# Optimization experiments

Hardware: AMD Instinct MI355X
Metric: run time of the kernel (lower is better)

## Reference

```python
import jax, jax.numpy as jnp
import numpy as np

B, S, M = 1, 1024, 1024          # batch, seq, hidden
H, D, KV = 16, 64, 8             # q heads, head dim, kv heads (kv hardcoded=8)
G = H // KV                      # gqa groups
FF = 3072                        # expert/shared mlp inner dim (hardcoded)
E, K = 64, 8                     # experts, topk (hardcoded)
CAP = 2 * K * S * B // E         # static expert capacity (>= dynamic max -> no drops)
RMS_EPS = 1e-6
F32_EPS = 1.1920929e-07          # torch.finfo(float32).eps


def _rms(x, w, eps=RMS_EPS):
    v = jnp.mean(x * x, axis=-1, keepdims=True)
    return w * (x * jax.lax.rsqrt(v + eps))


def _rotate_half(x):
    d = x.shape[-1] // 2
    return jnp.concatenate([-x[..., d:], x[..., :d]], axis=-1)


def _mlp(x, gu_w, dn_w):
    gu = x @ gu_w                       # [..., 2*FF]
    x1, x2 = gu[..., :FF], gu[..., FF:]
    return (x1 * jax.nn.silu(x2)) @ dn_w


def _topkgating(logits):
    # logits: [T, E] fp32
    gates = jax.nn.softmax(logits, axis=1)
    topv, topi = jax.lax.top_k(gates, K)                 # [T, K]
    gates_s = jnp.clip(jnp.sum(topv, axis=1, keepdims=True), F32_EPS)
    router_probs = gates / gates_s                        # [T, E]
    # priority: cumsum of one-hot over flattened (K, T) order, matching torch
    idx_flat = topi.T.reshape(-1)                         # [K*T]
    mask = jax.nn.one_hot(idx_flat, E, dtype=jnp.int32)   # [K*T, E]
    prio = jnp.cumsum(mask, axis=0) * mask - 1            # [K*T, E]
    prio = prio.reshape(K, -1, E).transpose(1, 0, 2).max(axis=1)  # [T, E]
    valid = (prio >= 0) & (prio < CAP)
    prio = jnp.where(valid, prio, 0)
    dispatch = jax.nn.one_hot(prio, CAP, dtype=jnp.float32) * valid[..., None]  # [T,E,C]
    combine = router_probs[..., None] * dispatch                                 # [T,E,C]
    return combine, dispatch


def setup_inputs() -> dict:
    key = jax.random.key(0)
    ks = jax.random.split(key, 10)
    sc = 0.02
    inv_freq = 1.0 / (10000.0 ** (jnp.arange(0, D, 2, dtype=jnp.float32) / D))
    t = jnp.arange(S, dtype=jnp.float32)
    freqs = jnp.outer(t, inv_freq)                        # [S, D/2]
    emb = jnp.concatenate([freqs, freqs], axis=-1)        # [S, D]
    cos = jnp.broadcast_to(jnp.cos(emb), (B, S, D))
    sin = jnp.broadcast_to(jnp.sin(emb), (B, S, D))
    return {
        'hidden_states': jax.random.normal(ks[0], (B, S, M), jnp.float32),
        'cos': cos,
        'sin': sin,
        'ln1_w': jnp.ones((M,), jnp.float32),
        'ln2_w': jnp.ones((M,), jnp.float32),
        'qkv_w': jax.random.normal(ks[1], (M, (H + 2 * KV) * D), jnp.float32) * sc,
        'o_w': jax.random.normal(ks[2], (H * D, M), jnp.float32) * sc,
        'qn_w': jnp.ones((D,), jnp.float32),
        'kn_w': jnp.ones((D,), jnp.float32),
        'shared_gu_w': jax.random.normal(ks[3], (M, 2 * FF), jnp.float32) * sc,
        'shared_dn_w': jax.random.normal(ks[4], (FF, M), jnp.float32) * sc,
        'gate_w': jax.random.normal(ks[5], (M, E), jnp.float32) * sc,
        'expert_gu_w': jax.random.normal(ks[6], (E, M, 2 * FF), jnp.float32) * sc,
        'expert_dn_w': jax.random.normal(ks[7], (E, FF, M), jnp.float32) * sc,
    }


def reference(hidden_states, cos, sin, ln1_w, ln2_w, qkv_w, o_w, qn_w, kn_w,
              shared_gu_w, shared_dn_w, gate_w, expert_gu_w, expert_dn_w):
    # ---- attention block ----
    hn = _rms(hidden_states, ln1_w)                       # input layernorm
    qkv = (hn @ qkv_w).reshape(B, S, KV, G + 2, D)
    q = qkv[..., :G, :].reshape(B, S, H, D).transpose(0, 2, 1, 3)   # [B,H,S,D]
    k = qkv[..., G, :].transpose(0, 2, 1, 3)                        # [B,KV,S,D]
    v = qkv[..., G + 1, :].transpose(0, 2, 1, 3)                    # [B,KV,S,D]
    c, s_ = cos[:, None], sin[:, None]                    # [B,1,S,D]
    q = q * c + _rotate_half(q) * s_
    k = k * c + _rotate_half(k) * s_
    q = _rms(q, qn_w)
    k = _rms(k, kn_w)
    k = jnp.repeat(k, G, axis=1)                          # GQA expand -> [B,H,S,D]
    v = jnp.repeat(v, G, axis=1)
    scores = jnp.einsum('bhqd,bhkd->bhqk', q, k) / np.sqrt(D)
    causal = jnp.tril(jnp.ones((S, S), bool))
    scores = jnp.where(causal, scores, -1e9)
    attn = jax.nn.softmax(scores, axis=-1)
    ao = jnp.einsum('bhqk,bhkd->bhqd', attn, v).transpose(0, 2, 1, 3).reshape(B, S, H * D)
    h = hidden_states + ao @ o_w                          # residual

    # ---- MoE block ----
    h2 = _rms(h, ln2_w)                                   # post-attn layernorm
    shared = _mlp(h2, shared_gu_w, shared_dn_w)           # [B,S,M]
    x = h2.reshape(-1, M)                                 # [T,M]
    logits = x @ gate_w                                   # fp32 gate
    combine, dispatch = _topkgating(logits)               # [T,E,C]
    dispatched = jnp.einsum('sec,sm->ecm', dispatch, x)   # [E,C,M]
    gu = jnp.einsum('ecm,emf->ecf', dispatched, expert_gu_w)  # [E,C,2*FF]
    x1, x2 = gu[..., :FF], gu[..., FF:]
    eo = jnp.einsum('ecf,efm->ecm', x1 * jax.nn.silu(x2), expert_dn_w)  # [E,C,M]
    combined = jnp.einsum('sec,ecm->sm', combine, eo).reshape(B, S, M)
    return h + shared + combined
```

## Files before the change

### kernel.cpp

```cpp
#include <hip/hip_runtime.h>

#define S 1024
#define MDIM 1024
#define NH 16
#define HD 64
#define NKV 8
#define FF 3072
#define NE 64
#define TOPK 8
#define CAP 256

typedef unsigned short u16;
typedef __attribute__((ext_vector_type(8))) short bf16x8;
typedef __attribute__((ext_vector_type(4))) float f32x4;

__device__ __forceinline__ u16 f2bf(float f) {
    union { float f; unsigned u; } x; x.f = f;
    unsigned r = x.u + 0x7FFFu + ((x.u >> 16) & 1u);
    return (u16)(r >> 16);
}
__device__ __forceinline__ float bf2f(u16 b) {
    union { unsigned u; float f; } x; x.u = ((unsigned)b) << 16;
    return x.f;
}
__device__ __forceinline__ void split1(float x, u16& h, u16& l) {
    h = f2bf(x);
    l = f2bf(x - bf2f(h));
}
__device__ __forceinline__ int swzcol(int row, int G) { return 8 * (G ^ ((row >> 3) & 3)); }

__device__ __forceinline__ void gl_lds16(const u16* g, u16* l) {
    __builtin_amdgcn_global_load_lds(
        (const __attribute__((address_space(1))) unsigned int*)g,
        (__attribute__((address_space(3))) unsigned int*)l, 16, 0, 0);
}

__global__ __launch_bounds__(256) void k_rms1(const float* __restrict__ x,
                                              const float* __restrict__ w,
                                              u16* __restrict__ ohi,
                                              u16* __restrict__ olo) {
    int s = blockIdx.x;
    const float* row = x + (size_t)s * MDIM;
    float v[4]; float ss = 0.f;
#pragma unroll
    for (int i = 0; i < 4; ++i) { v[i] = row[threadIdx.x + i * 256]; ss += v[i] * v[i]; }
#pragma unroll
    for (int of = 32; of; of >>= 1) ss += __shfl_xor(ss, of);
    __shared__ float red[4];
    int wid = threadIdx.x >> 6;
    if ((threadIdx.x & 63) == 0) red[wid] = ss;
    __syncthreads();
    float tot = red[0] + red[1] + red[2] + red[3];
    float sc = rsqrtf(tot * (1.f / MDIM) + 1e-6f);
#pragma unroll
    for (int i = 0; i < 4; ++i) {
        int c = threadIdx.x + i * 256;
        float ov = v[i] * sc * w[c];
        u16 hh, ll; split1(ov, hh, ll);
        ohi[(size_t)s * MDIM + c] = hh;
        olo[(size_t)s * MDIM + c] = ll;
    }
}

template <int EPI>
__global__ __launch_bounds__(256) void k_gemm_split(
    const u16* __restrict__ Ahi, const u16* __restrict__ Alo, int lda,
    const float* __restrict__ B, int ldb,
    float* __restrict__ C, int ldc,
    const float* __restrict__ resid, int M, int K) {
    int m0 = blockIdx.y * 64;
    int n0 = blockIdx.x * 64;
    __shared__ u16 Ah[2][64][32];
    __shared__ u16 Al[2][64][32];
    __shared__ u16 Bh[2][64][40];
    __shared__ u16 Bl[2][64][40];
    int tid = threadIdx.x, lane = tid & 63, wid = tid >> 6;
    int wm = (wid >> 1) * 32, wn = (wid & 1) * 32;
    f32x4 acc[2][2] = {};

    int rt = wid * 16 + (lane >> 2);
    int gsrc = (lane & 3) ^ ((lane >> 4) & 3);
    const u16* ahb = Ahi + (size_t)(m0 + rt) * lda + gsrc * 8;
    const u16* alb = Alo + (size_t)(m0 + rt) * lda + gsrc * 8;

    int nB = tid & 63, kbB = tid >> 6;
    int colB = swzcol(nB, kbB);
    float rb[8];
    auto loadB = [&](int k0) {
        const float* bp = B + (size_t)(k0 + kbB * 8) * ldb + n0 + nB;
#pragma unroll
        for (int i = 0; i < 8; ++i) rb[i] = bp[(size_t)i * ldb];
    };
    auto stageA = [&](int b, int k0) {
        gl_lds16(ahb + k0, &Ah[b][wid * 16][0]);
        gl_lds16(alb + k0, &Al[b][wid * 16][0]);
    };
    auto writeB = [&](int b) {
        bf16x8 hh, ll;
#pragma unroll
        for (int i = 0; i < 8; ++i) { u16 h, l; split1(rb[i], h, l); hh[i] = (short)h; ll[i] = (short)l; }
        *(bf16x8*)&Bh[b][nB][colB] = hh;
        *(bf16x8*)&Bl[b][nB][colB] = ll;
    };

    loadB(0); stageA(0, 0); writeB(0);
    __syncthreads();
    int NT = K / 32;
    for (int t = 0; t < NT; ++t) {
        int c = t & 1;
        if (t + 1 < NT) { loadB((t + 1) * 32); stageA(1 - c, (t + 1) * 32); }
        bf16x8 ah[2], al[2], bh[2], bl[2];
#pragma unroll
        for (int mi = 0; mi < 2; ++mi) {
            int r = wm + mi * 16 + (lane & 15);
            int cA = 8 * ((lane >> 4) ^ ((r >> 2) & 3));
            ah[mi] = *(const bf16x8*)&Ah[c][r][cA];
            al[mi] = *(const bf16x8*)&Al[c][r][cA];
        }
#pragma unroll
        for (int ni = 0; ni < 2; ++ni) {
            int r = wn + ni * 16 + (lane & 15);
            int cc = swzcol(r, lane >> 4);
            bh[ni] = *(const bf16x8*)&Bh[c][r][cc];
            bl[ni] = *(const bf16x8*)&Bl[c][r][cc];
        }
#pragma unroll
        for (int mi = 0; mi < 2; ++mi)
#pragma unroll
            for (int ni = 0; ni < 2; ++ni) {
                acc[mi][ni] = __builtin_amdgcn_mfma_f32_16x16x32_bf16(ah[mi], bh[ni], acc[mi][ni], 0, 0, 0);
                acc[mi][ni] = __builtin_amdgcn_mfma_f32_16x16x32_bf16(ah[mi], bl[ni], acc[mi][ni], 0, 0, 0);
                acc[mi][ni] = __builtin_amdgcn_mfma_f32_16x16x32_bf16(al[mi], bh[ni], acc[mi][ni], 0, 0, 0);
            }
        if (t + 1 < NT) { writeB(1 - c); __syncthreads(); }
    }
#pragma unroll
    for (int mi = 0; mi < 2; ++mi)
#pragma unroll
        for (int ni = 0; ni < 2; ++ni)
#pragma unroll
            for (int r = 0; r < 4; ++r) {
                int row = m0 + wm + mi * 16 + (lane >> 4) * 4 + r;
                int col = n0 + wn + ni * 16 + (lane & 15);
                float v = acc[mi][ni][r];
                if constexpr (EPI == 1) v += resid[(size_t)row * ldc + col];
                C[(size_t)row * ldc + col] = v;
            }
}

template <int TM, int TN, bool SWIGLU, bool XCD1D>
__global__ __launch_bounds__(256) void k_gemm_bf(
    const u16* __restrict__ A, int lda, long sAe,
    const float* __restrict__ B, long sBe, int ldb,
    u16* __restrict__ C, int ldc, long sCe,
    int K, int pairOff,
    const int* __restrict__ counts, const int* __restrict__ rowidx,
    const u16* __restrict__ Ash, const float* __restrict__ Bsh,
    u16* __restrict__ Csh, int Msh) {
    int z, byy, bxx;
    if constexpr (XCD1D) {
        int id = blockIdx.x;
        if (id < 1024) { byy = id >> 9; int t = id & 511; z = ((t >> 6) << 3) | (t & 7); bxx = (t >> 3) & 7; }
        else { int ms = id - 1024; z = NE + (ms >> 4); byy = (ms >> 3) & 1; bxx = ms & 7; }
    } else {
        z = blockIdx.z; byy = blockIdx.y; bxx = blockIdx.x;
    }
    int tid = threadIdx.x, lane = tid & 63, wid = tid >> 6;
    int M, m0;
    const int* ridx = nullptr;
    if (z >= NE) {
        int mslot = (z - NE) * 2 + byy;
        m0 = mslot * TM;
        M = Msh;
        A = Ash; B = Bsh; C = Csh;
        if (m0 >= M) return;
    } else {
        M = counts[z];
        m0 = byy * TM;
        if (m0 >= M) return;
        A += (size_t)z * sAe;
        B += (size_t)z * sBe;
        C += (size_t)z * sCe;
        if (rowidx) ridx = rowidx + z * CAP;
    }
    int n0 = bxx * TN;

    __shared__ u16 As[2][TM][32];
    __shared__ u16 Bs[2][TN][40];
    __shared__ u16 B2s[2][SWIGLU ? TN : 1][40];

    constexpr int MF = TM / 32;
    constexpr int NI = TN / 32;
    int wm = (wid >> 1) * (TM / 2), wn = (wid & 1) * (TN / 2);

    f32x4 acc[MF][NI] = {};
    f32x4 acc2[SWIGLU ? MF : 1][NI] = {};

    constexpr int NCH = TM / 16;
    constexpr int CPW = (NCH + 3) / 4;
    int arow_in = lane >> 2;
    int gsrc = (lane & 3) ^ ((lane >> 4) & 3);
    const u16* abase[CPW];
#pragma unroll
    for (int i = 0; i < CPW; ++i) {
        int ch = wid + i * 4;
        const u16* p = A;
        if (ch < NCH) {
            int rti = ch * 16 + arow_in;
            int gm = m0 + rti;
            long grow = (gm < M) ? (ridx ? (long)ridx[gm] : (long)gm) : 0;
            p = A + grow * (size_t)lda + gsrc * 8;
        }
        abase[i] = p;
    }
    auto stageA = [&](int b, int k0) {
#pragma unroll
        for (int i = 0; i < CPW; ++i) {
            int ch = wid + i * 4;
            if (ch < NCH) gl_lds16(abase[i] + k0, &As[b][ch * 16][0]);
        }
    };

    constexpr int NKG = 256 / TN;
    constexpr int OPT = 4 / NKG;
    int nB = tid % TN, kgB = tid / TN;
    float rb[OPT][8], rg[SWIGLU ? OPT : 1][8];
    auto loadB = [&](int k0) {
        const float* bp = B + (size_t)(k0 + kgB * OPT * 8) * ldb + n0 + nB;
#pragma unroll
        for (int j = 0; j < OPT; ++j)
#pragma unroll
            for (int i = 0; i < 8; ++i) {
                rb[j][i] = bp[(size_t)(j * 8 + i) * ldb];
                if constexpr (SWIGLU) rg[j][i] = bp[(size_t)(j * 8 + i) * ldb + pairOff];
            }
    };
    auto writeB = [&](int b) {
#pragma unroll
        for (int j = 0; j < OPT; ++j) {
            int col = swzcol(nB, kgB * OPT + j);
            bf16x8 v;
#pragma unroll
            for (int i = 0; i < 8; ++i) v[i] = (short)f2bf(rb[j][i]);
            *(bf16x8*)&Bs[b][nB][col] = v;
            if constexpr (SWIGLU) {
                bf16x8 g;
#pragma unroll
                for (int i = 0; i < 8; ++i) g[i] = (short)f2bf(rg[j][i]);
                *(bf16x8*)&B2s[b][nB][col] = g;
            }
        }
    };

    loadB(0); stageA(0, 0); writeB(0);
    __syncthreads();
    int NT = K / 32;
    for (int t = 0; t < NT; ++t) {
        int c = t & 1;
        if (t + 1 < NT) { loadB((t + 1) * 32); stageA(1 - c, (t + 1) * 32); }
        bf16x8 af[MF], bfr[NI], gfr[SWIGLU ? NI : 1];
#pragma unroll
        for (int mi = 0; mi < MF; ++mi) {
            int r = wm + mi * 16 + (lane & 15);
            int cA = 8 * ((lane >> 4) ^ ((r >> 2) & 3));
            af[mi] = *(const bf16x8*)&As[c][r][cA];
        }
#pragma unroll
        for (int ni = 0; ni < NI; ++ni) {
            int r = wn + ni * 16 + (lane & 15);
            int cB = swzcol(r, lane >> 4);
            bfr[ni] = *(const bf16x8*)&Bs[c][r][cB];
            if constexpr (SWIGLU) gfr[ni] = *(const bf16x8*)&B2s[c][r][cB];
        }
#pragma unroll
        for (int mi = 0; mi < MF; ++mi)
#pragma unroll
            for (int ni = 0; ni < NI; ++ni) {
                acc[mi][ni] = __builtin_amdgcn_mfma_f32_16x16x32_bf16(af[mi], bfr[ni], acc[mi][ni], 0, 0, 0);
                if constexpr (SWIGLU)
                    acc2[mi][ni] = __builtin_amdgcn_mfma_f32_16x16x32_bf16(af[mi], gfr[ni], acc2[mi][ni], 0, 0, 0);
            }
        if (t + 1 < NT) { writeB(1 - c); __syncthreads(); }
    }
#pragma unroll
    for (int mi = 0; mi < MF; ++mi)
#pragma unroll
        for (int ni = 0; ni < NI; ++ni)
#pragma unroll
            for (int r = 0; r < 4; ++r) {
                int row = m0 + wm + mi * 16 + (lane >> 4) * 4 + r;
                int col = n0 + wn + ni * 16 + (lane & 15);
                if (row >= M) continue;
                float x1 = acc[mi][ni][r];
                if constexpr (SWIGLU) {
                    float x2 = acc2[mi][ni][r];
                    x1 = x1 * (x2 / (1.f + __expf(-x2)));
                }
                C[(size_t)row * ldc + col] = f2bf(x1);
            }
}

__global__ __launch_bounds__(256) void k_rope(const float* __restrict__ qkv,
                                              const float* __restrict__ cosb,
                                              const float* __restrict__ sinb,
                                              const float* __restrict__ qn_w,
                                              const float* __restrict__ kn_w,
                                              u16* __restrict__ qh, u16* __restrict__ ql,
                                              u16* __restrict__ kh, u16* __restrict__ kl,
                                              u16* __restrict__ vh, u16* __restrict__ vl) {
    int wid = threadIdx.x >> 6, lane = threadIdx.x & 63;
    int idx = blockIdx.x * 4 + wid;
    int s = idx >> 3, j = idx & 7;
    const float* base = qkv + (size_t)s * 2048 + j * 256;
    float c = cosb[s * HD + lane], sn = sinb[s * HD + lane];
    u16 hh, ll;
    split1(base[192 + lane], hh, ll);
    vh[((size_t)j * S + s) * HD + lane] = hh;
    vl[((size_t)j * S + s) * HD + lane] = ll;
#pragma unroll
    for (int r = 0; r < 3; ++r) {
        float x = base[r * 64 + lane];
        float xp = __shfl_xor(x, 32);
        float rot = (lane < 32) ? -xp : xp;
        float y = x * c + rot * sn;
        float ss = y * y;
#pragma unroll
        for (int o = 32; o; o >>= 1) ss += __shfl_xor(ss, o);
        float scale = rsqrtf(ss * (1.f / 64.f) + 1e-6f);
        float outv = y * scale * ((r == 2) ? kn_w[lane] : qn_w[lane]);
        split1(outv, hh, ll);
        if (r == 2) {
            kh[((size_t)j * S + s) * HD + lane] = hh;
            kl[((size_t)j * S + s) * HD + lane] = ll;
        } else {
            qh[((size_t)(j * 2 + r) * S + s) * HD + lane] = hh;
            ql[((size_t)(j * 2 + r) * S + s) * HD + lane] = ll;
        }
    }
}

__global__ __launch_bounds__(256) void k_attn(const u16* __restrict__ qh, const u16* __restrict__ ql,
                                              const u16* __restrict__ kmh, const u16* __restrict__ kml,
                                              const u16* __restrict__ vmh, const u16* __restrict__ vml,
                                              u16* __restrict__ aoh, u16* __restrict__ aol) {
    int qt = 15 - blockIdx.x;
    int h = blockIdx.y;
    int q0 = qt * 64;
    size_t qoff = (size_t)h * S * HD;
    size_t koff = (size_t)(h >> 1) * S * HD;
    size_t voff = koff;

    __shared__ u16 Vh[64][72];
    __shared__ u16 Vl[64][72];
    __shared__ u16 Ph_l[4][16][72];
    __shared__ u16 Pl_l[4][16][72];

    int tid = threadIdx.x, lane = tid & 63, w = tid >> 6;
    int rgrp = lane >> 4;
    int l16 = lane & 15;

    bf16x8 qfh[2], qfl[2];
#pragma unroll
    for (int ks = 0; ks < 2; ++ks) {
        size_t o = qoff + (size_t)(q0 + w * 16 + l16) * HD + ks * 32 + rgrp * 8;
        qfh[ks] = *(const bf16x8*)(qh + o);
        qfl[ks] = *(const bf16x8*)(ql + o);
    }

    float m_[4], l_[4];
    f32x4 o_[4] = {};
#pragma unroll
    for (int r = 0; r < 4; ++r) { m_[r] = -1e30f; l_[r] = 0.f; }

    for (int kt = 0; kt <= qt; ++kt) {
        int kc = kt * 64;
#pragma unroll
        for (int i = 0; i < 16; ++i) {
            int idx = tid + i * 256;
            int kr = idx >> 6, d = idx & 63;
            Vh[d][kr] = vmh[voff + (size_t)(kc + kr) * HD + d];
            Vl[d][kr] = vml[voff + (size_t)(kc + kr) * HD + d];
        }
        __syncthreads();

        f32x4 sacc[4] = {};
#pragma unroll
        for (int ks = 0; ks < 2; ++ks) {
            bf16x8 bh[4], bl[4];
#pragma unroll
            for (int ni = 0; ni < 4; ++ni) {
                size_t o = koff + (size_t)(kc + ni * 16 + l16) * HD + ks * 32 + rgrp * 8;
                bh[ni] = *(const bf16x8*)(kmh + o);
                bl[ni] = *(const bf16x8*)(kml + o);
            }
#pragma unroll
            for (int ni = 0; ni < 4; ++ni) {
                sacc[ni] = __builtin_amdgcn_mfma_f32_16x16x32_bf16(qfh[ks], bh[ni], sacc[ni], 0, 0, 0);
                sacc[ni] = __builtin_amdgcn_mfma_f32_16x16x32_bf16(qfh[ks], bl[ni], sacc[ni], 0, 0, 0);
                sacc[ni] = __builtin_amdgcn_mfma_f32_16x16x32_bf16(qfl[ks], bh[ni], sacc[ni], 0, 0, 0);
            }
        }
#pragma unroll
        for (int ni = 0; ni < 4; ++ni)
#pragma unroll
            for (int r = 0; r < 4; ++r) {
                int qrow = q0 + w * 16 + rgrp * 4 + r;
                int col = kc + ni * 16 + l16;
                float sv = sacc[ni][r] * 0.125f;
                sacc[ni][r] = (col > qrow) ? -1e30f : sv;
            }
        float pm[4], mnew[4], sf[4], ps[4];
#pragma unroll
        for (int r = 0; r < 4; ++r) {
            float mx = fmaxf(fmaxf(sacc[0][r], sacc[1][r]), fmaxf(sacc[2][r], sacc[3][r]));
#pragma unroll
            for (int off = 1; off < 16; off <<= 1) mx = fmaxf(mx, __shfl_xor(mx, off));
            pm[r] = mx;
            mnew[r] = fmaxf(m_[r], pm[r]);
            sf[r] = __expf(m_[r] - mnew[r]);
            m_[r] = mnew[r];
            ps[r] = 0.f;
        }
#pragma unroll
        for (int ni = 0; ni < 4; ++ni)
#pragma unroll
            for (int r = 0; r < 4; ++r) {
                float p = __expf(sacc[ni][r] - mnew[r]);
                ps[r] += p;
                u16 hh, ll; split1(p, hh, ll);
                Ph_l[w][rgrp * 4 + r][ni * 16 + l16] = hh;
                Pl_l[w][rgrp * 4 + r][ni * 16 + l16] = ll;
            }
#pragma unroll
        for (int r = 0; r < 4; ++r) {
            float s_ = ps[r];
#pragma unroll
            for (int off = 1; off < 16; off <<= 1) s_ += __shfl_xor(s_, off);
            l_[r] = l_[r] * sf[r] + s_;
        }
#pragma unroll
        for (int ni = 0; ni < 4; ++ni)
#pragma unroll
            for (int r = 0; r < 4; ++r) o_[ni][r] *= sf[r];
#pragma unroll
        for (int ks2 = 0; ks2 < 2; ++ks2) {
            bf16x8 pah = *(const bf16x8*)&Ph_l[w][l16][ks2 * 32 + rgrp * 8];
            bf16x8 pal = *(const bf16x8*)&Pl_l[w][l16][ks2 * 32 + rgrp * 8];
            bf16x8 vbh[4], vbl[4];
#pragma unroll
            for (int ni = 0; ni < 4; ++ni) {
                vbh[ni] = *(const bf16x8*)&Vh[ni * 16 + l16][ks2 * 32 + rgrp * 8];
                vbl[ni] = *(const bf16x8*)&Vl[ni * 16 + l16][ks2 * 32 + rgrp * 8];
            }
#pragma unroll
            for (int ni = 0; ni < 4; ++ni) {
                o_[ni] = __builtin_amdgcn_mfma_f32_16x16x32_bf16(pah, vbh[ni], o_[ni], 0, 0, 0);
                o_[ni] = __builtin_amdgcn_mfma_f32_16x16x32_bf16(pah, vbl[ni], o_[ni], 0, 0, 0);
                o_[ni] = __builtin_amdgcn_mfma_f32_16x16x32_bf16(pal, vbh[ni], o_[ni], 0, 0, 0);
            }
        }
        __syncthreads();
    }
#pragma unroll
    for (int r = 0; r < 4; ++r) {
        float inv = 1.f / l_[r];
        int row = q0 + w * 16 + rgrp * 4 + r;
#pragma unroll
        for (int ni = 0; ni < 4; ++ni) {
            float val = o_[ni][r] * inv;
            u16 hh, ll; split1(val, hh, ll);
            size_t o = (size_t)row * MDIM + h * HD + ni * 16 + l16;
            aoh[o] = hh;
            aol[o] = ll;
        }
    }
}

__global__ __launch_bounds__(256) void k_rms2_router(const float* __restrict__ h,
                                                     const float* __restrict__ w,
                                                     const float* __restrict__ gw,
                                                     u16* __restrict__ h2b,
                                                     int* __restrict__ topi,
                                                     float* __restrict__ wts) {
    __shared__ float xr[1024];
    __shared__ float part[4][64];
    __shared__ float red[4];
    int s = blockIdx.x, tid = threadIdx.x;
    const float* row = h + (size_t)s * MDIM;
    float v[4]; float ss = 0.f;
#pragma unroll
    for (int i = 0; i < 4; ++i) { v[i] = row[tid + i * 256]; ss += v[i] * v[i]; }
#pragma unroll
    for (int of = 32; of; of >>= 1) ss += __shfl_xor(ss, of);
    if ((tid & 63) == 0) red[tid >> 6] = ss;
    __syncthreads();
    float tot = red[0] + red[1] + red[2] + red[3];
    float sc = rsqrtf(tot * (1.f / MDIM) + 1e-6f);
#pragma unroll
    for (int i = 0; i < 4; ++i) {
        int c = tid + i * 256;
        float ov = v[i] * sc * w[c];
        xr[c] = ov;
        h2b[(size_t)s * MDIM + c] = f2bf(ov);
    }
    __syncthreads();
    int e = tid & 63, qq = tid >> 6;
    float acc = 0.f;
    for (int i = 0; i < 256; ++i) acc += xr[qq * 256 + i] * gw[(size_t)(qq * 256 + i) * NE + e];
    part[qq][e] = acc;
    __syncthreads();
    if (tid < 64) {
        int lane = tid;
        float lg = part[0][lane] + part[1][lane] + part[2][lane] + part[3][lane];
        float mx = lg;
#pragma unroll
        for (int o = 32; o; o >>= 1) mx = fmaxf(mx, __shfl_xor(mx, o));
        float ex = __expf(lg - mx);
        float sum = ex;
#pragma unroll
        for (int o = 32; o; o >>= 1) sum += __shfl_xor(sum, o);
        float g = ex / sum;
        float cur = g;
        float tv[TOPK]; int ti[TOPK];
        float tsum = 0.f;
#pragma unroll
        for (int k = 0; k < TOPK; ++k) {
            float vv = cur; int ii = lane;
#pragma unroll
            for (int o = 32; o; o >>= 1) {
                float vo = __shfl_xor(vv, o);
                int io = __shfl_xor(ii, o);
                if (vo > vv || (vo == vv && io < ii)) { vv = vo; ii = io; }
            }
            tv[k] = vv; ti[k] = ii; tsum += vv;
            if (lane == ii) cur = -1.f;
        }
        float gs = fmaxf(tsum, 1.1920929e-07f);
        if (lane == 0) {
#pragma unroll
            for (int k = 0; k < TOPK; ++k) {
                topi[s * TOPK + k] = ti[k];
                wts[s * TOPK + k] = tv[k] / gs;
            }
        }
    }
}

__global__ __launch_bounds__(512) void k_slots(const int* __restrict__ topi, int* __restrict__ slots,
                                               int* __restrict__ counts, int* __restrict__ etok) {
    __shared__ int tl[S * TOPK];
    __shared__ int cnt[TOPK][NE];
    __shared__ int base[TOPK][NE];
    int tid = threadIdx.x;
    for (int i = tid; i < S * TOPK; i += 512) tl[i] = topi[i];
    ((int*)cnt)[tid] = 0;
    __syncthreads();
    for (int i = tid; i < S * TOPK; i += 512)
        atomicAdd(&cnt[i & 7][tl[i]], 1);
    __syncthreads();
    if (tid < NE) {
        int acc = 0;
#pragma unroll
        for (int k = 0; k < TOPK; ++k) { base[k][tid] = acc; acc += cnt[k][tid]; }
        counts[tid] = acc < CAP ? acc : CAP;
    }
    __syncthreads();
    int k = tid >> 6, e = tid & 63;
    int rank = base[k][e];
    for (int s = 0; s < S; ++s) {
        if (tl[s * TOPK + k] == e) {
            if (rank < CAP) { slots[s * TOPK + k] = rank; etok[e * CAP + rank] = s; }
            else slots[s * TOPK + k] = -1;
            rank++;
        }
    }
}

__global__ __launch_bounds__(256) void k_combine(const float* __restrict__ h,
                                                 const u16* __restrict__ sh,
                                                 const u16* __restrict__ eo,
                                                 const int* __restrict__ topi,
                                                 const int* __restrict__ slots,
                                                 const float* __restrict__ wts,
                                                 float* __restrict__ out) {
    int s = blockIdx.x, t = threadIdx.x;
    float w[TOPK]; int off[TOPK];
#pragma unroll
    for (int k = 0; k < TOPK; ++k) {
        int sl = slots[s * TOPK + k];
        int ee = topi[s * TOPK + k];
        w[k] = wts[s * TOPK + k];
        off[k] = (sl >= 0) ? ee * CAP + sl : -1;
    }
#pragma unroll
    for (int i = 0; i < 4; ++i) {
        int col = t + i * 256;
        float acc = h[(size_t)s * MDIM + col] + bf2f(sh[(size_t)s * MDIM + col]);
#pragma unroll
        for (int k = 0; k < TOPK; ++k)
            if (off[k] >= 0) acc += w[k] * bf2f(eo[(size_t)off[k] * MDIM + col]);
        out[(size_t)s * MDIM + col] = acc;
    }
}

extern "C" void kernel_launch(void* const* d_in, const int* in_sizes, int n_in,
                              void* d_out, int out_size, void* d_ws, size_t ws_size,
                              hipStream_t stream) {
    (void)in_sizes; (void)n_in; (void)out_size; (void)ws_size;
    const float* hidden = (const float*)d_in[0];
    const float* cosb   = (const float*)d_in[1];
    const float* sinb   = (const float*)d_in[2];
    const float* ln1_w  = (const float*)d_in[3];
    const float* ln2_w  = (const float*)d_in[4];
    const float* qkv_w  = (const float*)d_in[5];
    const float* o_w    = (const float*)d_in[6];
    const float* qn_w   = (const float*)d_in[7];
    const float* kn_w   = (const float*)d_in[8];
    const float* sgu_w  = (const float*)d_in[9];
    const float* sdn_w  = (const float*)d_in[10];
    const float* gate_w = (const float*)d_in[11];
    const float* egu_w  = (const float*)d_in[12];
    const float* edn_w  = (const float*)d_in[13];
    float* out = (float*)d_out;

    char* ws = (char*)d_ws;
    size_t off = 0;
    auto alloc = [&](size_t bytes) -> void* {
        void* p = ws + off;
        off = (off + bytes + 255) & ~(size_t)255;
        return p;
    };
    u16*   hn_hi   = (u16*)  alloc((size_t)S * MDIM * 2);
    u16*   hn_lo   = (u16*)  alloc((size_t)S * MDIM * 2);
    float* qkvb    = (float*)alloc((size_t)S * 2048 * 4);
    u16*   qhb     = (u16*)  alloc((size_t)NH * S * HD * 2);
    u16*   qlb     = (u16*)  alloc((size_t)NH * S * HD * 2);
    u16*   khb     = (u16*)  alloc((size_t)NKV * S * HD * 2);
    u16*   klb     = (u16*)  alloc((size_t)NKV * S * HD * 2);
    u16*   vhb     = (u16*)  alloc((size_t)NKV * S * HD * 2);
    u16*   vlb     = (u16*)  alloc((size_t)NKV * S * HD * 2);
    u16*   ao_hi   = (u16*)  alloc((size_t)S * MDIM * 2);
    u16*   ao_lo   = (u16*)  alloc((size_t)S * MDIM * 2);
    float* hbuf    = (float*)alloc((size_t)S * MDIM * 4);
    u16*   h2b     = (u16*)  alloc((size_t)S * MDIM * 2);
    u16*   gatedS  = (u16*)  alloc((size_t)S * FF * 2);
    u16*   sharedO = (u16*)  alloc((size_t)S * MDIM * 2);
    int*   topi    = (int*)  alloc((size_t)S * TOPK * 4);
    float* wts     = (float*)alloc((size_t)S * TOPK * 4);
    int*   slots   = (int*)  alloc((size_t)S * TOPK * 4);
    int*   counts  = (int*)  alloc((size_t)NE * 4);
    int*   etok    = (int*)  alloc((size_t)NE * CAP * 4);
    u16*   egated  = (u16*)  alloc((size_t)NE * CAP * FF * 2);
    u16*   eo      = (u16*)  alloc((size_t)NE * CAP * MDIM * 2);

    k_rms1<<<dim3(S), 256, 0, stream>>>(hidden, ln1_w, hn_hi, hn_lo);
    k_gemm_split<0><<<dim3(2048 / 64, S / 64), 256, 0, stream>>>(
        hn_hi, hn_lo, MDIM, qkv_w, 2048, qkvb, 2048, nullptr, S, MDIM);
    k_rope<<<dim3(S * NKV / 4), 256, 0, stream>>>(qkvb, cosb, sinb, qn_w, kn_w,
                                                  qhb, qlb, khb, klb, vhb, vlb);
    k_attn<<<dim3(16, NH), 256, 0, stream>>>(qhb, qlb, khb, klb, vhb, vlb, ao_hi, ao_lo);
    k_gemm_split<1><<<dim3(MDIM / 64, S / 64), 256, 0, stream>>>(
        ao_hi, ao_lo, MDIM, o_w, MDIM, hbuf, MDIM, hidden, S, MDIM);
    k_rms2_router<<<dim3(S), 256, 0, stream>>>(hbuf, ln2_w, gate_w, h2b, topi, wts);
    k_slots<<<dim3(1), 512, 0, stream>>>(topi, slots, counts, etok);
    k_gemm_bf<160, 64, true, false><<<dim3(FF / 64, 2, NE + 4), 256, 0, stream>>>(
        h2b, MDIM, 0, egu_w, (long)MDIM * 2 * FF, 2 * FF,
        egated, FF, (long)CAP * FF, MDIM, FF, counts, etok,
        h2b, sgu_w, gatedS, S);
    k_gemm_bf<160, 128, false, true><<<dim3(1088, 1, 1), 256, 0, stream>>>(
        egated, FF, (long)CAP * FF, edn_w, (long)FF * MDIM, MDIM,
        eo, MDIM, (long)CAP * MDIM, FF, 0, counts, nullptr,
        gatedS, sdn_w, sharedO, S);
    k_combine<<<dim3(S), 256, 0, stream>>>(hbuf, sharedO, eo, topi, slots, wts, out);
}
```

Measured before the change: 902.7 us.

## Prefetch B two tiles ahead with manual vmcnt waits in expert GEMM

Restructures the k-loop of the bf16 expert GEMM so the fp32 B operand is loaded into registers two k-tiles ahead, alternating between two register sets, while A is staged one tile ahead. Hand-written s_waitcnt vmcnt counts and sched barriers replace the compiler's conservative waits, so global-load latency overlaps the MFMA compute. This costs extra VGPRs for the second B buffer, and the hardcoded vmcnt constants assume TM=160 and a fixed per-wave load count, which makes them fragile if the tile shape or load pattern changes.

Measured after the change: 1.474 ms. +63.3%, slower.

```diff
diff --git a/kernel.cpp b/kernel.cpp
--- a/kernel.cpp
+++ b/kernel.cpp
@@ -157,6 +157,7 @@
     const int* __restrict__ counts, const int* __restrict__ rowidx,
     const u16* __restrict__ Ash, const float* __restrict__ Bsh,
     u16* __restrict__ Csh, int Msh) {
+    static_assert(TM == 160, "vmcnt constants assume TM=160 (A gload_lds ops per wave in {2,3})");
     int z, byy, bxx;
     if constexpr (XCD1D) {
         int id = blockIdx.x;
@@ -224,8 +225,11 @@
     constexpr int NKG = 256 / TN;
     constexpr int OPT = 4 / NKG;
     int nB = tid % TN, kgB = tid / TN;
-    float rb[OPT][8], rg[SWIGLU ? OPT : 1][8];
-    auto loadB = [&](int k0) {
+    typedef float rb_t[OPT][8];
+    typedef float rg_t[SWIGLU ? OPT : 1][8];
+    rb_t rbA, rbB;
+    rg_t rgA, rgB;
+    auto loadB = [&](int k0, rb_t& rb, rg_t& rg) {
         const float* bp = B + (size_t)(k0 + kgB * OPT * 8) * ldb + n0 + nB;
 #pragma unroll
         for (int j = 0; j < OPT; ++j)
@@ -235,7 +239,7 @@
                 if constexpr (SWIGLU) rg[j][i] = bp[(size_t)(j * 8 + i) * ldb + pairOff];
             }
     };
-    auto writeB = [&](int b) {
+    auto writeB = [&](int b, rb_t& rb, rg_t& rg) {
 #pragma unroll
         for (int j = 0; j < OPT; ++j) {
             int col = swzcol(nB, kgB * OPT + j);
@@ -251,13 +255,7 @@
             }
         }
     };
-
-    loadB(0); stageA(0, 0); writeB(0);
-    __syncthreads();
-    int NT = K / 32;
-    for (int t = 0; t < NT; ++t) {
-        int c = t & 1;
-        if (t + 1 < NT) { loadB((t + 1) * 32); stageA(1 - c, (t + 1) * 32); }
+    auto compute = [&](int c) {
         bf16x8 af[MF], bfr[NI], gfr[SWIGLU ? NI : 1];
 #pragma unroll
         for (int mi = 0; mi < MF; ++mi) {
@@ -280,7 +278,39 @@
                 if constexpr (SWIGLU)
                     acc2[mi][ni] = __builtin_amdgcn_mfma_f32_16x16x32_bf16(af[mi], gfr[ni], acc2[mi][ni], 0, 0, 0);
             }
-        if (t + 1 < NT) { writeB(1 - c); __syncthreads(); }
+    };
+    auto step = [&](int t, int c, int o, rb_t& rbQ, rg_t& rgQ, rb_t& rbP, rg_t& rgP, int NT) {
+        if (t + 1 < NT) stageA(o, (t + 1) * 32);
+        bool haveQ = (t + 2 < NT);
+        if (haveQ) loadB((t + 2) * 32, rbQ, rgQ);
+        compute(c);
+        if (t + 1 < NT) {
+            if (haveQ) asm volatile("s_waitcnt vmcnt(18)" ::: "memory");
+            else       asm volatile("s_waitcnt vmcnt(2)"  ::: "memory");
+            __builtin_amdgcn_sched_barrier(0);
+            writeB(o, rbP, rgP);
+            if (haveQ) asm volatile("s_waitcnt vmcnt(16)" ::: "memory");
+            else       asm volatile("s_waitcnt vmcnt(0)"  ::: "memory");
+            asm volatile("s_waitcnt lgkmcnt(0)" ::: "memory");
+            __builtin_amdgcn_sched_barrier(0);
+            __builtin_amdgcn_s_barrier();
+            __builtin_amdgcn_sched_barrier(0);
+        }
+    };
+
+    int NT = K / 32;
+    stageA(0, 0);
+    loadB(0, rbA, rgA);
+    asm volatile("s_waitcnt vmcnt(0)" ::: "memory");
+    __builtin_amdgcn_sched_barrier(0);
+    writeB(0, rbA, rgA);
+    if (1 < NT) loadB(32, rbB, rgB);
+    asm volatile("s_waitcnt lgkmcnt(0)" ::: "memory");
+    __builtin_amdgcn_s_barrier();
+    __builtin_amdgcn_sched_barrier(0);
+    for (int t = 0; t < NT; t += 2) {
+        step(t,     0, 1, rbA, rgA, rbB, rgB, NT);
+        step(t + 1, 1, 0, rbB, rgB, rbA, rgA, NT);
     }
 #pragma unroll
     for (int mi = 0; mi < MF; ++mi)
```

## Replace LDS-staged down-projection GEMM with register-direct MFMA kernel

Applied to the files above, without the earlier changes.

Adds a new GEMM kernel for the expert and shared down-projection that skips LDS staging. Each wave loads its A fragments and the fp32 B weights straight from global memory into registers, converts them to bf16 and issues MFMAs, which removes shared-memory writes and barriers. Each wave now covers all TM rows for its own column slice, so nothing is shared between waves and A is re-read by every wave. The B loads are strided scalar loads along ldb, which risks poor coalescing and no latency hiding from double buffering.

Result: slower. 1.147 ms (+27.1%).

```diff
diff --git a/kernel.cpp b/kernel.cpp
--- a/kernel.cpp
+++ b/kernel.cpp
@@ -148,7 +148,7 @@
             }
 }
 
-template <int TM, int TN, bool SWIGLU, bool XCD1D>
+template <int TM, int TN, bool SWIGLU>
 __global__ __launch_bounds__(256) void k_gemm_bf(
     const u16* __restrict__ A, int lda, long sAe,
     const float* __restrict__ B, long sBe, int ldb,
@@ -157,14 +157,7 @@
     const int* __restrict__ counts, const int* __restrict__ rowidx,
     const u16* __restrict__ Ash, const float* __restrict__ Bsh,
     u16* __restrict__ Csh, int Msh) {
-    int z, byy, bxx;
-    if constexpr (XCD1D) {
-        int id = blockIdx.x;
-        if (id < 1024) { byy = id >> 9; int t = id & 511; z = ((t >> 6) << 3) | (t & 7); bxx = (t >> 3) & 7; }
-        else { int ms = id - 1024; z = NE + (ms >> 4); byy = (ms >> 3) & 1; bxx = ms & 7; }
-    } else {
-        z = blockIdx.z; byy = blockIdx.y; bxx = blockIdx.x;
-    }
+    int z = blockIdx.z, byy = blockIdx.y, bxx = blockIdx.x;
     int tid = threadIdx.x, lane = tid & 63, wid = tid >> 6;
     int M, m0;
     const int* ridx = nullptr;
@@ -297,6 +290,84 @@
                     x1 = x1 * (x2 / (1.f + __expf(-x2)));
                 }
                 C[(size_t)row * ldc + col] = f2bf(x1);
+            }
+}
+
+template <int TM, int TN>
+__global__ __launch_bounds__(256) void k_gemm_reg(
+    const u16* __restrict__ A, int lda, long sAe,
+    const float* __restrict__ B, long sBe, int ldb,
+    u16* __restrict__ C, int ldc, long sCe,
+    int K,
+    const int* __restrict__ counts,
+    const u16* __restrict__ Ash, const float* __restrict__ Bsh,
+    u16* __restrict__ Csh, int Msh) {
+    int id = blockIdx.x;
+    int z, byy, bxx;
+    if (id < 1024) { byy = id >> 9; int t = id & 511; z = ((t >> 6) << 3) | (t & 7); bxx = (t >> 3) & 7; }
+    else { int ms = id - 1024; z = NE + (ms >> 4); byy = (ms >> 3) & 1; bxx = ms & 7; }
+    int tid = threadIdx.x, lane = tid & 63, w = tid >> 6;
+    int M, m0;
+    if (z >= NE) {
+        int mslot = (z - NE) * 2 + byy;
+        m0 = mslot * TM;
+        M = Msh;
+        A = Ash; B = Bsh; C = Csh;
+        if (m0 >= M) return;
+    } else {
+        M = counts[z];
+        m0 = byy * TM;
+        if (m0 >= M) return;
+        A += (size_t)z * sAe;
+        B += (size_t)z * sBe;
+        C += (size_t)z * sCe;
+    }
+    int n0 = bxx * TN;
+    constexpr int MF = TM / 16;
+    constexpr int NI = TN / 64;
+    int rgrp = lane >> 4, l16 = lane & 15;
+    int wn = n0 + w * (TN / 4);
+
+    f32x4 acc[MF][NI] = {};
+    const u16* ab[MF];
+#pragma unroll
+    for (int mi = 0; mi < MF; ++mi)
+        ab[mi] = A + (size_t)(m0 + mi * 16 + l16) * lda + rgrp * 8;
+    const float* bb[NI];
+#pragma unroll
+    for (int ni = 0; ni < NI; ++ni)
+        bb[ni] = B + (size_t)(rgrp * 8) * ldb + wn + ni * 16 + l16;
+
+    int NT = K / 32;
+    for (int t = 0; t < NT; ++t) {
+        bf16x8 bf[NI];
+#pragma unroll
+        for (int ni = 0; ni < NI; ++ni) {
+            const float* bp = bb[ni] + (size_t)t * 32 * ldb;
+            bf16x8 v;
+#pragma unroll
+            for (int i = 0; i < 8; ++i) v[i] = (short)f2bf(bp[(size_t)i * ldb]);
+            bf[ni] = v;
+        }
+        bf16x8 af[MF];
+#pragma unroll
+        for (int mi = 0; mi < MF; ++mi) af[mi] = *(const bf16x8*)(ab[mi] + t * 32);
+#pragma unroll
+        for (int mi = 0; mi < MF; ++mi)
+#pragma unroll
+            for (int ni = 0; ni < NI; ++ni)
+                acc[mi][ni] = __builtin_amdgcn_mfma_f32_16x16x32_bf16(af[mi], bf[ni], acc[mi][ni], 0, 0, 0);
+    }
+#pragma unroll
+    for (int mi = 0; mi < MF; ++mi)
+#pragma unroll
+        for (int ni = 0; ni < NI; ++ni)
+#pragma unroll
+            for (int r = 0; r < 4; ++r) {
+                int row = m0 + mi * 16 + rgrp * 4 + r;
+                if (row >= M) continue;
+                int col = wn + ni * 16 + l16;
+                C[(size_t)row * ldc + col] = f2bf(acc[mi][ni][r]);
             }
 }
 
@@ -663,13 +734,13 @@
         ao_hi, ao_lo, MDIM, o_w, MDIM, hbuf, MDIM, hidden, S, MDIM);
     k_rms2_router<<<dim3(S), 256, 0, stream>>>(hbuf, ln2_w, gate_w, h2b, topi, wts);
     k_slots<<<dim3(1), 512, 0, stream>>>(topi, slots, counts, etok);
-    k_gemm_bf<160, 64, true, false><<<dim3(FF / 64, 2, NE + 4), 256, 0, stream>>>(
+    k_gemm_bf<160, 64, true><<<dim3(FF / 64, 2, NE + 4), 256, 0, stream>>>(
         h2b, MDIM, 0, egu_w, (long)MDIM * 2 * FF, 2 * FF,
         egated, FF, (long)CAP * FF, MDIM, FF, counts, etok,
         h2b, sgu_w, gatedS, S);
-    k_gemm_bf<160, 128, false, true><<<dim3(1088, 1, 1), 256, 0, stream>>>(
+    k_gemm_reg<160, 128><<<dim3(1088, 1, 1), 256, 0, stream>>>(
         egated, FF, (long)CAP * FF, edn_w, (long)FF * MDIM, MDIM,
-        eo, MDIM, (long)CAP * MDIM, FF, 0, counts, nullptr,
+        eo, MDIM, (long)CAP * MDIM, FF, counts,
         gatedS, sdn_w, sharedO, S);
     k_combine<<<dim3(S), 256, 0, stream>>>(hbuf, sharedO, eo, topi, slots, wts, out);
 }
```
